# Performance work log

Measured on AMD Instinct MI355X. Metric: run time of the kernel, lower is better.

## Reference

```python
import jax, jax.numpy as jnp
import numpy as np
import math

B, N, D, H, K = 8, 256, 128, 256, 128


def setup_inputs() -> dict:
    key = jax.random.key(0)
    ks = jax.random.split(key, 8)
    # forward args
    x = jax.random.uniform(ks[0], (B, N, N), dtype=jnp.float32) * 3.0  # pairwise distances
    atom_embeds = jax.random.normal(ks[1], (B, N, D), dtype=jnp.float32)
    # params of nn.Linear(2D, H) and nn.Linear(H, 2) (store as [in, out])
    lim1 = 1.0 / math.sqrt(2 * D)
    W1 = jax.random.uniform(ks[2], (2 * D, H), minval=-lim1, maxval=lim1, dtype=jnp.float32)
    b1 = jax.random.uniform(ks[3], (H,), minval=-lim1, maxval=lim1, dtype=jnp.float32)
    lim2 = 1.0 / math.sqrt(H)
    W2 = jax.random.uniform(ks[4], (H, 2), minval=-lim2, maxval=lim2, dtype=jnp.float32)
    b2 = jax.random.uniform(ks[5], (2,), minval=-lim2, maxval=lim2, dtype=jnp.float32)
    # RBF params: means ~ U(0,3), temps ~ U(0.1,10)
    means = jax.random.uniform(ks[6], (K,), minval=0.0, maxval=3.0, dtype=jnp.float32)
    temps = jax.random.uniform(ks[7], (K,), minval=0.1, maxval=10.0, dtype=jnp.float32)
    return {"x": x, "atom_embeds": atom_embeds, "W1": W1, "b1": b1,
            "W2": W2, "b2": b2, "means": means, "temps": temps}


def reference(x, atom_embeds, W1, b1, W2, b2, means, temps):
    d = atom_embeds.shape[-1]
    scale = 1.0 / math.sqrt(2 * d)
    # Split-weight trick: cat([e_i, e_j]) @ W1 == e_i @ W1[:D] + e_j @ W1[D:]
    # (same math, avoids materializing the [B,N,N,2D] concat)
    hi = jnp.einsum('bnd,dh->bnh', atom_embeds, W1[:d])   # [B,N,H]
    hj = jnp.einsum('bnd,dh->bnh', atom_embeds, W1[d:])   # [B,N,H]
    h = jax.nn.relu(hi[:, :, None, :] + hj[:, None, :, :] + b1)  # [B,N,N,H]
    edge_features = (jnp.einsum('bijh,ho->bijo', h, W2) + b2) * scale  # [B,N,N,2]
    mul = edge_features[..., 0:1]   # [B,N,N,1]
    bias = edge_features[..., 1:2]  # [B,N,N,1]
    v = mul * x[..., None] + bias   # [B,N,N,1]
    temp = jnp.abs(temps)
    # RBF gaussian basis expansion -> [B,N,N,K]
    return jnp.exp(-jnp.square(v - means) * temp)
```

## Files before the change

kernel.cpp:

```cpp
#include <hip/hip_runtime.h>
#include <hip/hip_bf16.h>


#define NB 8
#define NN 256
#define ND 128
#define NH 256
#define NK 128
#define GI 2

__global__ __launch_bounds__(256) void precompute_hij(
    const float* __restrict__ atom, const float* __restrict__ W1,
    const float* __restrict__ b1,
    float* __restrict__ hi, float* __restrict__ hjbT) {
  const int h = threadIdx.x;
  const int base = blockIdx.x * 8;
  const int b  = base >> 8;
  const int j0 = base & 255;
  __shared__ float a[8][ND];
  for (int t = threadIdx.x; t < 8 * ND; t += 256) {
    a[t >> 7][t & 127] = atom[(size_t)base * ND + t];
  }
  __syncthreads();
  float acc0[8], acc1[8];
  const float bv = b1[h];
#pragma unroll
  for (int r = 0; r < 8; ++r) { acc0[r] = 0.f; acc1[r] = bv; }
  for (int d = 0; d < ND; ++d) {
    const float w0 = W1[d * NH + h];
    const float w1 = W1[(ND + d) * NH + h];
#pragma unroll
    for (int r = 0; r < 8; ++r) {
      acc0[r] = fmaf(a[r][d], w0, acc0[r]);
      acc1[r] = fmaf(a[r][d], w1, acc1[r]);
    }
  }
#pragma unroll
  for (int r = 0; r < 8; ++r) {
    hi[(size_t)(base + r) * NH + h] = acc0[r];
    hjbT[((size_t)b * NH + h) * NN + (j0 + r)] = acc1[r];
  }
}

__global__ __launch_bounds__(256) void edge_rbf(
    const float* __restrict__ x,
    const float* __restrict__ hi, const float* __restrict__ hjbT,
    const float* __restrict__ W2, const float* __restrict__ b2,
    const float* __restrict__ means, const float* __restrict__ temps,
    float* __restrict__ out) {
  const int b    = blockIdx.x & 7;
  const int i0   = (blockIdx.x >> 3) * GI;
  const int lane = threadIdx.x & 63;
  const int wave = threadIdx.x >> 6;

  __shared__ float part0[4][GI][NN];
  __shared__ float part1[4][GI][NN];
  __shared__ float vsh[GI][NN];

  const float* __restrict__ hjrow  = hjbT + ((size_t)b * NH + wave * 64) * NN;
  const float* __restrict__ w2row  = W2 + wave * 128;
  const float* __restrict__ hibase = hi + ((size_t)(b * NN + i0)) * NH + wave * 64;

  float acc0[GI][4], acc1[GI][4];
#pragma unroll
  for (int r = 0; r < GI; ++r)
#pragma unroll
    for (int q = 0; q < 4; ++q) { acc0[r][q] = 0.f; acc1[r][q] = 0.f; }

#pragma unroll 8
  for (int hh = 0; hh < 64; ++hh) {
    const float4 hj4 = *reinterpret_cast<const float4*>(hjrow + (size_t)hh * NN + 4 * lane);
    const float w0 = w2row[2 * hh];
    const float w1 = w2row[2 * hh + 1];
#pragma unroll
    for (int r = 0; r < GI; ++r) {
      const float hih = hibase[(size_t)r * NH + hh];
      const float a0 = fmaxf(hih + hj4.x, 0.f);
      const float a1 = fmaxf(hih + hj4.y, 0.f);
      const float a2 = fmaxf(hih + hj4.z, 0.f);
      const float a3 = fmaxf(hih + hj4.w, 0.f);
      acc0[r][0] = fmaf(a0, w0, acc0[r][0]); acc1[r][0] = fmaf(a0, w1, acc1[r][0]);
      acc0[r][1] = fmaf(a1, w0, acc0[r][1]); acc1[r][1] = fmaf(a1, w1, acc1[r][1]);
      acc0[r][2] = fmaf(a2, w0, acc0[r][2]); acc1[r][2] = fmaf(a2, w1, acc1[r][2]);
      acc0[r][3] = fmaf(a3, w0, acc0[r][3]); acc1[r][3] = fmaf(a3, w1, acc1[r][3]);
    }
  }
#pragma unroll
  for (int r = 0; r < GI; ++r) {
    *reinterpret_cast<float4*>(&part0[wave][r][4 * lane]) =
        make_float4(acc0[r][0], acc0[r][1], acc0[r][2], acc0[r][3]);
    *reinterpret_cast<float4*>(&part1[wave][r][4 * lane]) =
        make_float4(acc1[r][0], acc1[r][1], acc1[r][2], acc1[r][3]);
  }
  __syncthreads();

  {
    const int t = threadIdx.x;
    const float scale = 0.0625f;
    const float b20 = b2[0], b21 = b2[1];
#pragma unroll
    for (int r = 0; r < GI; ++r) {
      const float s0 = part0[0][r][t] + part0[1][r][t] + part0[2][r][t] + part0[3][r][t];
      const float s1 = part1[0][r][t] + part1[1][r][t] + part1[2][r][t] + part1[3][r][t];
      const float mul  = (s0 + b20) * scale;
      const float bias = (s1 + b21) * scale;
      vsh[r][t] = fmaf(mul, x[(size_t)(b * NN + i0 + r) * NN + t], bias);
    }
  }
  __syncthreads();

  const int k0 = (lane & 31) * 4;
  const int jhalf = lane >> 5;
  const float LOG2E = 1.44269504088896340736f;
  const float4 mv = *reinterpret_cast<const float4*>(means + k0);
  float4 tv = *reinterpret_cast<const float4*>(temps + k0);
  tv.x = -fabsf(tv.x) * LOG2E;
  tv.y = -fabsf(tv.y) * LOG2E;
  tv.z = -fabsf(tv.z) * LOG2E;
  tv.w = -fabsf(tv.w) * LOG2E;

#pragma unroll
  for (int r = 0; r < GI; ++r) {
    float* __restrict__ orow = out + ((size_t)(b * NN + i0 + r) * NN + wave * 64) * NK;
#pragma unroll 4
    for (int c = 0; c < 32; ++c) {
      const int j = 2 * c + jhalf;
      const float vj = vsh[r][wave * 64 + j];
      const float d0 = vj - mv.x;
      const float d1 = vj - mv.y;
      const float d2 = vj - mv.z;
      const float d3 = vj - mv.w;
      float4 e;
      e.x = __builtin_amdgcn_exp2f(d0 * d0 * tv.x);
      e.y = __builtin_amdgcn_exp2f(d1 * d1 * tv.y);
      e.z = __builtin_amdgcn_exp2f(d2 * d2 * tv.z);
      e.w = __builtin_amdgcn_exp2f(d3 * d3 * tv.w);
      *reinterpret_cast<float4*>(orow + (size_t)j * NK + k0) = e;
    }
  }
}

extern "C" void kernel_launch(void* const* d_in, const int* in_sizes, int n_in,
                              void* d_out, int out_size, void* d_ws, size_t ws_size,
                              hipStream_t stream) {
  const float* x     = (const float*)d_in[0];
  const float* atom  = (const float*)d_in[1];
  const float* W1    = (const float*)d_in[2];
  const float* b1    = (const float*)d_in[3];
  const float* W2    = (const float*)d_in[4];
  const float* b2    = (const float*)d_in[5];
  const float* means = (const float*)d_in[6];
  const float* temps = (const float*)d_in[7];
  float* out = (float*)d_out;

  float* hi   = (float*)d_ws;
  float* hjbT = hi + (size_t)NB * NN * NH;

  precompute_hij<<<NB * NN / 8, 256, 0, stream>>>(atom, W1, b1, hi, hjbT);
  edge_rbf<<<NB * NN / GI, 256, 0, stream>>>(x, hi, hjbT, W2, b2, means, temps, out);
}
```

Measured before the change: 73.33 us.

## Split edge kernel into v computation and separate streaming RBF store kernel

The fused edge kernel is split into two. compute_v writes the per-edge scalar v to a workspace buffer. A new rbf_store kernel then expands each v into 128 Gaussian basis values with a flat, fully coalesced float4 store pattern strided across the whole output. The aim is to decouple the compute-bound MLP part from the store-bound 134MB output write so the store phase gets full occupancy and streaming writes. The cost is an extra kernel launch and a small global round-trip for v.

```diff
diff --git a/kernel.cpp b/kernel.cpp
--- a/kernel.cpp
+++ b/kernel.cpp
@@ -8,6 +8,8 @@
 #define NH 256
 #define NK 128
 #define GI 2
+
+typedef float f32x4 __attribute__((ext_vector_type(4)));
 
 __global__ __launch_bounds__(256) void precompute_hij(
     const float* __restrict__ atom, const float* __restrict__ W1,
@@ -42,12 +44,11 @@
   }
 }
 
-__global__ __launch_bounds__(256) void edge_rbf(
+__global__ __launch_bounds__(256) void compute_v(
     const float* __restrict__ x,
     const float* __restrict__ hi, const float* __restrict__ hjbT,
     const float* __restrict__ W2, const float* __restrict__ b2,
-    const float* __restrict__ means, const float* __restrict__ temps,
-    float* __restrict__ out) {
+    float* __restrict__ v) {
   const int b    = blockIdx.x & 7;
   const int i0   = (blockIdx.x >> 3) * GI;
   const int lane = threadIdx.x & 63;
@@ -55,7 +56,6 @@
 
   __shared__ float part0[4][GI][NN];
   __shared__ float part1[4][GI][NN];
-  __shared__ float vsh[GI][NN];
 
   const float* __restrict__ hjrow  = hjbT + ((size_t)b * NH + wave * 64) * NN;
   const float* __restrict__ w2row  = W2 + wave * 128;
@@ -104,39 +104,43 @@
       const float s1 = part1[0][r][t] + part1[1][r][t] + part1[2][r][t] + part1[3][r][t];
       const float mul  = (s0 + b20) * scale;
       const float bias = (s1 + b21) * scale;
-      vsh[r][t] = fmaf(mul, x[(size_t)(b * NN + i0 + r) * NN + t], bias);
+      const size_t bij = (size_t)(b * NN + i0 + r) * NN + t;
+      v[bij] = fmaf(mul, x[bij], bias);
     }
   }
-  __syncthreads();
+}
 
-  const int k0 = (lane & 31) * 4;
-  const int jhalf = lane >> 5;
+__global__ __launch_bounds__(256) void rbf_store(
+    const float* __restrict__ v,
+    const float* __restrict__ means, const float* __restrict__ temps,
+    float* __restrict__ out) {
+  const int idx = blockIdx.x * 256 + threadIdx.x;
+  const int k0  = (idx & 31) * 4;
+
   const float LOG2E = 1.44269504088896340736f;
   const float4 mv = *reinterpret_cast<const float4*>(means + k0);
   float4 tv = *reinterpret_cast<const float4*>(temps + k0);
-  tv.x = -fabsf(tv.x) * LOG2E;
-  tv.y = -fabsf(tv.y) * LOG2E;
-  tv.z = -fabsf(tv.z) * LOG2E;
-  tv.w = -fabsf(tv.w) * LOG2E;
+  const float t0 = -fabsf(tv.x) * LOG2E;
+  const float t1 = -fabsf(tv.y) * LOG2E;
+  const float t2 = -fabsf(tv.z) * LOG2E;
+  const float t3 = -fabsf(tv.w) * LOG2E;
 
-#pragma unroll
-  for (int r = 0; r < GI; ++r) {
-    float* __restrict__ orow = out + ((size_t)(b * NN + i0 + r) * NN + wave * 64) * NK;
+  const float* __restrict__ vp = v + (idx >> 5);
+  float* __restrict__ op = out + (size_t)idx * 4;
+
 #pragma unroll 4
-    for (int c = 0; c < 32; ++c) {
-      const int j = 2 * c + jhalf;
-      const float vj = vsh[r][wave * 64 + j];
-      const float d0 = vj - mv.x;
-      const float d1 = vj - mv.y;
-      const float d2 = vj - mv.z;
-      const float d3 = vj - mv.w;
-      float4 e;
-      e.x = __builtin_amdgcn_exp2f(d0 * d0 * tv.x);
-      e.y = __builtin_amdgcn_exp2f(d1 * d1 * tv.y);
-      e.z = __builtin_amdgcn_exp2f(d2 * d2 * tv.z);
-      e.w = __builtin_amdgcn_exp2f(d3 * d3 * tv.w);
-      *reinterpret_cast<float4*>(orow + (size_t)j * NK + k0) = e;
-    }
+  for (int s = 0; s < 32; ++s) {
+    const float vj = vp[s * 16384];
+    const float d0 = vj - mv.x;
+    const float d1 = vj - mv.y;
+    const float d2 = vj - mv.z;
+    const float d3 = vj - mv.w;
+    f32x4 e;
+    e.x = __builtin_amdgcn_exp2f(d0 * d0 * t0);
+    e.y = __builtin_amdgcn_exp2f(d1 * d1 * t1);
+    e.z = __builtin_amdgcn_exp2f(d2 * d2 * t2);
+    e.w = __builtin_amdgcn_exp2f(d3 * d3 * t3);
+    *reinterpret_cast<f32x4*>(op + (size_t)s * 2097152) = e;
   }
 }
 
@@ -155,7 +159,9 @@
 
   float* hi   = (float*)d_ws;
   float* hjbT = hi + (size_t)NB * NN * NH;
+  float* v    = hjbT + (size_t)NB * NH * NN;
 
   precompute_hij<<<NB * NN / 8, 256, 0, stream>>>(atom, W1, b1, hi, hjbT);
-  edge_rbf<<<NB * NN / GI, 256, 0, stream>>>(x, hi, hjbT, W2, b2, means, temps, out);
+  compute_v<<<NB * NN / GI, 256, 0, stream>>>(x, hi, hjbT, W2, b2, v);
+  rbf_store<<<2048, 256, 0, stream>>>(v, means, temps, out);
 }
```

After: 84.93 us. 15.8% more time.
